# Optimization experiments

Hardware: AMD Instinct MI355X
Metric: run time of the kernel (lower is better)

## Reference

```python
import jax, jax.numpy as jnp
import numpy as np

G_NUMS = 30      # group_nums
G_SIZE = 100     # group_size (also neighborhood_size)
BETA = 1.0
EPS = 1e-9


def setup_inputs() -> dict:
    key = jax.random.key(0)
    pointclouds = jax.random.normal(key, (8, 131072, 3), dtype=jnp.float32)
    return {"pointclouds": pointclouds}


def _knn_gather(points, queries, k):
    """points [b,N,3], queries [b,G,3] -> k nearest points per query [b,G,k,3]."""
    # squared distances [b,G,N]
    d2 = (
        jnp.sum(queries * queries, axis=-1)[..., None]
        - 2.0 * jnp.einsum("bgd,bnd->bgn", queries, points)
        + jnp.sum(points * points, axis=-1)[:, None, :]
    )
    _, idx = jax.lax.top_k(-d2, k)                    # [b,G,k]
    nbrs = jax.vmap(lambda p, i: p[i])(points, idx)   # [b,G,k,3]
    return nbrs


def reference(pointclouds):
    b, N, _ = pointclouds.shape
    # --- group_points: uniform-stride sampled centers, k-NN groups, group means ---
    stride = N // G_NUMS
    centers = pointclouds[:, ::stride][:, :G_NUMS]                 # [b,G,3]
    grouped = _knn_gather(pointclouds, centers, G_SIZE)            # [b,G,K,3]
    group_means = jnp.mean(grouped, axis=2)                        # [b,G,3]

    # --- estimate_pointcloud_local_coord_frames: per-group 3x3 PCA ---
    nbrs = _knn_gather(pointclouds, group_means, G_SIZE)           # [b,G,K,3]
    mu = jnp.mean(nbrs, axis=2, keepdims=True)
    X = nbrs - mu
    cov = jnp.einsum("bgkd,bgke->bgde", X, X) / G_SIZE             # [b,G,3,3]
    curvatures, frames = jnp.linalg.eigh(cov)                      # eigvals ascending

    # --- elongated-shape loss ---
    denom = curvatures[..., 0] + curvatures[..., 1] + curvatures[..., 2] + EPS
    first_vec = curvatures[..., 2] / denom
    second_vec = curvatures[..., 1] / denom
    elongated_shape_loss = -jnp.sum(first_vec - second_vec) / b

    # --- angular smoothness cost over group means / principal directions ---
    dirs = frames[..., :, 2]                                       # [b,G,3] largest-eig direction
    dm = jnp.sum(
        (group_means[:, :, None, :] - group_means[:, None, :, :]) ** 2, axis=-1
    )                                                              # [b,G,G]
    dm = dm + jnp.eye(G_NUMS, dtype=dm.dtype) * jnp.float32(1e30)  # exclude self
    j = jnp.argmin(dm, axis=-1)                                    # [b,G]
    dirs_j = jnp.take_along_axis(dirs, j[..., None], axis=1)       # [b,G,3]
    cos = jnp.sum(dirs * dirs_j, axis=-1)
    dlo_smooth_loss = jnp.mean(1.0 - cos * cos)                    # sign-invariant angle cost

    return elongated_shape_loss + BETA * dlo_smooth_loss
```

## Files before the change

kernel.cpp:

```cpp
#include <hip/hip_runtime.h>
#include <math.h>

#define N_PTS     131072
#define G_NUMS    30
#define G_SIZE    100
#define PT_STRIDE (N_PTS / G_NUMS)
#define TPB       1024
#define NWAVES    (TPB / 64)
#define BINS      4096
#define JB        (BINS / TPB)
#define SHIFT     20
#define SAMPLE_GRPS 1024
#define RANK_CUT  32
#define CAP       3072
#define TIE_CAP   64

struct KSmem {
    union {
        unsigned hist[BINS];
        struct {
            float gm[256][3];
            float dir[256][3];
            float pe[NWAVES];
            float ps[NWAVES];
        } fin;
    };
    unsigned wsum[NWAVES];
    unsigned T;
    int ns, nd, nt;
    unsigned u[CAP];
    int idx[CAP];
    float px[CAP], py[CAP], pz[CAP];
    int sel[G_SIZE];
    unsigned tu[TIE_CAP];
    int ti[TIE_CAP];
    float acc[3], cov[6], q[3];
    unsigned tau0, maxu, r1;
    float delta2;
};

__device__ __forceinline__ float dist2f(float px, float py, float pz,
                                        float qx, float qy, float qz) {
    float dx = px - qx, dy = py - qy, dz = pz - qz;
    return fmaf(dx, dx, fmaf(dy, dy, dz * dz));
}

__device__ __forceinline__ unsigned find_bin(KSmem& sm, unsigned rank,
                                             int tid, int lane, int wid) {
    unsigned hv[JB], csum = 0;
#pragma unroll
    for (int j = 0; j < JB; j++) { hv[j] = sm.hist[tid * JB + j]; csum += hv[j]; }
    unsigned inc = csum;
#pragma unroll
    for (int off = 1; off < 64; off <<= 1) {
        unsigned n = __shfl_up(inc, off);
        if (lane >= off) inc += n;
    }
    __syncthreads();
    if (lane == 63) sm.wsum[wid] = inc;
    __syncthreads();
    unsigned base = 0;
    for (int w = 0; w < wid; w++) base += sm.wsum[w];
    unsigned c = base + inc - csum;
#pragma unroll
    for (int j = 0; j < JB; j++) {
        if (c < rank && c + hv[j] >= rank) sm.T = (unsigned)(tid * JB + j);
        c += hv[j];
    }
    __syncthreads();
    return sm.T;
}

__device__ __forceinline__ void push4(KSmem& sm, const float4& xv, const float4& yv,
                                      const float4& zv, int i, unsigned tau,
                                      float qx, float qy, float qz) {
    unsigned u0 = __float_as_uint(dist2f(xv.x, yv.x, zv.x, qx, qy, qz));
    unsigned u1 = __float_as_uint(dist2f(xv.y, yv.y, zv.y, qx, qy, qz));
    unsigned u2 = __float_as_uint(dist2f(xv.z, yv.z, zv.z, qx, qy, qz));
    unsigned u3 = __float_as_uint(dist2f(xv.w, yv.w, zv.w, qx, qy, qz));
    int i0 = i * 4;
    if (u0 < tau) { int p = atomicAdd(&sm.ns, 1); if (p < CAP) { sm.u[p] = u0; sm.idx[p] = i0;     sm.px[p] = xv.x; sm.py[p] = yv.x; sm.pz[p] = zv.x; } }
    if (u1 < tau) { int p = atomicAdd(&sm.ns, 1); if (p < CAP) { sm.u[p] = u1; sm.idx[p] = i0 + 1; sm.px[p] = xv.y; sm.py[p] = yv.y; sm.pz[p] = zv.y; } }
    if (u2 < tau) { int p = atomicAdd(&sm.ns, 1); if (p < CAP) { sm.u[p] = u2; sm.idx[p] = i0 + 2; sm.px[p] = xv.z; sm.py[p] = yv.z; sm.pz[p] = zv.z; } }
    if (u3 < tau) { int p = atomicAdd(&sm.ns, 1); if (p < CAP) { sm.u[p] = u3; sm.idx[p] = i0 + 3; sm.px[p] = xv.w; sm.py[p] = yv.w; sm.pz[p] = zv.w; } }
}

template<bool SOA>
__device__ void knn_select(const float4* __restrict__ P4,
                           const float4* __restrict__ X4,
                           const float4* __restrict__ Y4,
                           const float4* __restrict__ Z4,
                           KSmem& sm, float qx, float qy, float qz,
                           int tid, int lane, int wid, bool save_tau) {
    for (int j = tid; j < BINS; j += TPB) sm.hist[j] = 0u;
    if (tid == 0) { sm.ns = 0; sm.nd = 0; sm.nt = 0; sm.T = 0u; }
    __syncthreads();

    if constexpr (SOA) {
        for (int i = tid; i < SAMPLE_GRPS; i += TPB) {
            float4 xv = X4[i], yv = Y4[i], zv = Z4[i];
            atomicAdd(&sm.hist[__float_as_uint(dist2f(xv.x, yv.x, zv.x, qx, qy, qz)) >> SHIFT], 1u);
            atomicAdd(&sm.hist[__float_as_uint(dist2f(xv.y, yv.y, zv.y, qx, qy, qz)) >> SHIFT], 1u);
            atomicAdd(&sm.hist[__float_as_uint(dist2f(xv.z, yv.z, zv.z, qx, qy, qz)) >> SHIFT], 1u);
            atomicAdd(&sm.hist[__float_as_uint(dist2f(xv.w, yv.w, zv.w, qx, qy, qz)) >> SHIFT], 1u);
        }
    } else {
        for (int grp = tid; grp < SAMPLE_GRPS; grp += TPB) {
            float4 f0 = P4[3 * grp + 0];
            float4 f1 = P4[3 * grp + 1];
            float4 f2 = P4[3 * grp + 2];
            atomicAdd(&sm.hist[__float_as_uint(dist2f(f0.x, f0.y, f0.z, qx, qy, qz)) >> SHIFT], 1u);
            atomicAdd(&sm.hist[__float_as_uint(dist2f(f0.w, f1.x, f1.y, qx, qy, qz)) >> SHIFT], 1u);
            atomicAdd(&sm.hist[__float_as_uint(dist2f(f1.z, f1.w, f2.x, qx, qy, qz)) >> SHIFT], 1u);
            atomicAdd(&sm.hist[__float_as_uint(dist2f(f2.y, f2.z, f2.w, qx, qy, qz)) >> SHIFT], 1u);
        }
    }
    __syncthreads();
    unsigned Tc = find_bin(sm, RANK_CUT, tid, lane, wid);
    const unsigned tau = (Tc >= BINS - 1) ? 0xFFFFFFFFu : ((Tc + 1) << SHIFT);
    if (save_tau && tid == 0) sm.tau0 = tau;
    for (int j = tid; j < BINS; j += TPB) sm.hist[j] = 0u;
    __syncthreads();

    if constexpr (SOA) {
        for (int base = 0; base < N_PTS / 4; base += TPB * 4) {
            int ia = base + tid, ib = ia + TPB, ic = ib + TPB, id_ = ic + TPB;
            float4 xa = X4[ia], ya = Y4[ia], za = Z4[ia];
            float4 xb = X4[ib], yb = Y4[ib], zb = Z4[ib];
            float4 xc = X4[ic], yc = Y4[ic], zc = Z4[ic];
            float4 xd = X4[id_], yd = Y4[id_], zd = Z4[id_];
            push4(sm, xa, ya, za, ia, tau, qx, qy, qz);
            push4(sm, xb, yb, zb, ib, tau, qx, qy, qz);
            push4(sm, xc, yc, zc, ic, tau, qx, qy, qz);
            push4(sm, xd, yd, zd, id_, tau, qx, qy, qz);
        }
    } else {
#pragma unroll 4
        for (int grp = tid; grp < N_PTS / 4; grp += TPB) {
            float4 f0 = P4[3 * grp + 0];
            float4 f1 = P4[3 * grp + 1];
            float4 f2 = P4[3 * grp + 2];
            float4 xv = make_float4(f0.x, f0.w, f1.z, f2.y);
            float4 yv = make_float4(f0.y, f1.x, f1.w, f2.z);
            float4 zv = make_float4(f0.z, f1.y, f2.x, f2.w);
            push4(sm, xv, yv, zv, grp, tau, qx, qy, qz);
        }
    }
    __syncthreads();
    int S = sm.ns; if (S > CAP) S = CAP;

    unsigned hb = 32u - (unsigned)__clz(tau - 1u);
    unsigned s2 = hb > 12u ? hb - 12u : 0u;
    for (int i = tid; i < S; i += TPB) atomicAdd(&sm.hist[sm.u[i] >> s2], 1u);
    __syncthreads();
    unsigned T2 = find_bin(sm, G_SIZE, tid, lane, wid);
    const unsigned lo = T2 << s2;

    for (int i = tid; i < S; i += TPB) {
        unsigned uu = sm.u[i];
        if (uu < lo) {
            int p = atomicAdd(&sm.nd, 1);
            if (p < G_SIZE) sm.sel[p] = i;
        } else if ((uu >> s2) == T2) {
            int p = atomicAdd(&sm.nt, 1);
            if (p < TIE_CAP) { sm.tu[p] = uu; sm.ti[p] = i; }
        }
    }
    __syncthreads();
    if (tid == 0) {
        int nd = sm.nd; if (nd > G_SIZE) nd = G_SIZE;
        int need = G_SIZE - nd;
        int ec = sm.nt; if (ec > TIE_CAP) ec = TIE_CAP;
        for (int a = 0; a < need && a < ec; ++a) {
            int best = a;
            for (int j = a + 1; j < ec; ++j)
                if (sm.tu[j] < sm.tu[best] ||
                    (sm.tu[j] == sm.tu[best] && sm.idx[sm.ti[j]] < sm.idx[sm.ti[best]])) best = j;
            unsigned tub = sm.tu[best]; sm.tu[best] = sm.tu[a]; sm.tu[a] = tub;
            int tib = sm.ti[best]; sm.ti[best] = sm.ti[a]; sm.ti[a] = tib;
            sm.sel[nd + a] = sm.ti[a];
        }
    }
    __syncthreads();
}

__device__ void eig3(const float cf[6], double lam_out[3], double dir_out[3]) {
    double a[3][3], v[3][3];
    a[0][0] = cf[0]; a[0][1] = cf[1]; a[0][2] = cf[2];
    a[1][0] = cf[1]; a[1][1] = cf[3]; a[1][2] = cf[4];
    a[2][0] = cf[2]; a[2][1] = cf[4]; a[2][2] = cf[5];
    for (int i = 0; i < 3; i++)
        for (int j = 0; j < 3; j++) v[i][j] = (i == j) ? 1.0 : 0.0;

    for (int sweep = 0; sweep < 12; sweep++) {
        double off = a[0][1] * a[0][1] + a[0][2] * a[0][2] + a[1][2] * a[1][2];
        if (off == 0.0) break;
        for (int p = 0; p < 2; p++) {
            for (int q = p + 1; q < 3; q++) {
                double apq = a[p][q];
                if (apq == 0.0) continue;
                double app = a[p][p], aqq = a[q][q];
                double theta = (aqq - app) / (2.0 * apq);
                double t = (theta >= 0.0 ? 1.0 : -1.0) /
                           (fabs(theta) + sqrt(theta * theta + 1.0));
                double c = 1.0 / sqrt(t * t + 1.0);
                double s = t * c;
                a[p][p] = app - t * apq;
                a[q][q] = aqq + t * apq;
                a[p][q] = 0.0; a[q][p] = 0.0;
                for (int r = 0; r < 3; r++) {
                    if (r == p || r == q) continue;
                    double arp = a[r][p], arq = a[r][q];
                    a[r][p] = c * arp - s * arq; a[p][r] = a[r][p];
                    a[r][q] = s * arp + c * arq; a[q][r] = a[r][q];
                }
                for (int r = 0; r < 3; r++) {
                    double vrp = v[r][p], vrq = v[r][q];
                    v[r][p] = c * vrp - s * vrq;
                    v[r][q] = s * vrp + c * vrq;
                }
            }
        }
    }
    double l0 = a[0][0], l1 = a[1][1], l2 = a[2][2];
    int i0 = 0, i1 = 1, i2 = 2;
    if (l0 > l1) { double t = l0; l0 = l1; l1 = t; int ti = i0; i0 = i1; i1 = ti; }
    if (l1 > l2) { double t = l1; l1 = l2; l2 = t; int ti = i1; i1 = i2; i2 = ti; }
    if (l0 > l1) { double t = l0; l0 = l1; l1 = t; int ti = i0; i0 = i1; i1 = ti; }
    lam_out[0] = l0; lam_out[1] = l1; lam_out[2] = l2;
    dir_out[0] = v[0][i2]; dir_out[1] = v[1][i2]; dir_out[2] = v[2][i2];
}

template<bool SOA>
__global__ __launch_bounds__(TPB)
void fused_knn_kernel(const float* __restrict__ pts,
                      const float* __restrict__ sx, const float* __restrict__ sy,
                      const float* __restrict__ sz,
                      float* __restrict__ gmeans, float* __restrict__ covs,
                      float* __restrict__ out,
                      unsigned* __restrict__ syncw,
                      int B, int nblk) {
    __shared__ KSmem sm;
    __shared__ int s_fastok;
    __shared__ int s_last;

    const int blk = blockIdx.x;
    const int b = blk % B;
    const int g = blk / B;
    const int gi = b * G_NUMS + g;
    const float* __restrict__ P = pts + (size_t)b * (N_PTS * 3);
    const float4* __restrict__ P4 = (const float4*)P;
    const float4* X4 = nullptr; const float4* Y4 = nullptr; const float4* Z4 = nullptr;
    if constexpr (SOA) {
        X4 = (const float4*)(sx + (size_t)b * N_PTS);
        Y4 = (const float4*)(sy + (size_t)b * N_PTS);
        Z4 = (const float4*)(sz + (size_t)b * N_PTS);
    }
    const int tid = threadIdx.x;
    const int lane = tid & 63, wid = tid >> 6;

    if (tid == 0) {
        const float* qp = P + (size_t)g * PT_STRIDE * 3;
        sm.q[0] = qp[0]; sm.q[1] = qp[1]; sm.q[2] = qp[2];
    }
    if (tid < 3) sm.acc[tid] = 0.f;
    if (tid < 6) sm.cov[tid] = 0.f;
    __syncthreads();
    const float qx = sm.q[0], qy = sm.q[1], qz = sm.q[2];

    knn_select<SOA>(P4, X4, Y4, Z4, sm, qx, qy, qz, tid, lane, wid, true);

    if (tid < G_SIZE) {
        int p = sm.sel[tid];
        atomicAdd(&sm.acc[0], sm.px[p]);
        atomicAdd(&sm.acc[1], sm.py[p]);
        atomicAdd(&sm.acc[2], sm.pz[p]);
    }
    __syncthreads();
    const int S0 = sm.ns;
    if (tid == 0) {
        float mx = sm.acc[0] * (1.0f / G_SIZE);
        float my = sm.acc[1] * (1.0f / G_SIZE);
        float mz = sm.acc[2] * (1.0f / G_SIZE);
        gmeans[(size_t)gi * 3 + 0] = mx;
        gmeans[(size_t)gi * 3 + 1] = my;
        gmeans[(size_t)gi * 3 + 2] = mz;
        float dx = mx - qx, dy = my - qy, dz = mz - qz;
        sm.delta2 = fmaf(dx, dx, fmaf(dy, dy, dz * dz));
        sm.q[0] = mx; sm.q[1] = my; sm.q[2] = mz;
        sm.acc[0] = 0.f; sm.acc[1] = 0.f; sm.acc[2] = 0.f;
        sm.maxu = 0u; sm.r1 = 0u; sm.T = 0u;
        sm.nd = 0; sm.nt = 0;
        s_last = 0;
        s_fastok = 0;
    }
    __syncthreads();
    const float q1x = sm.q[0], q1y = sm.q[1], q1z = sm.q[2];

    const bool attempt = (S0 >= G_SIZE) && (S0 <= CAP);
    if (attempt) {
        for (int j = tid; j < BINS; j += TPB) sm.hist[j] = 0u;
        for (int i = tid; i < S0; i += TPB) {
            unsigned uu = __float_as_uint(
                dist2f(sm.px[i], sm.py[i], sm.pz[i], q1x, q1y, q1z));
            sm.u[i] = uu;
            atomicMax(&sm.maxu, uu);
        }
        __syncthreads();
        unsigned maxu = sm.maxu;
        unsigned hb = (maxu == 0u) ? 0u : (32u - (unsigned)__clz(maxu));
        unsigned s3 = hb > 12u ? hb - 12u : 0u;
        for (int i = tid; i < S0; i += TPB) atomicAdd(&sm.hist[sm.u[i] >> s3], 1u);
        __syncthreads();
        unsigned T2 = find_bin(sm, G_SIZE, tid, lane, wid);
        const unsigned lo = T2 << s3;
        for (int i = tid; i < S0; i += TPB) {
            unsigned uu = sm.u[i];
            if (uu < lo) {
                int p = atomicAdd(&sm.nd, 1);
                if (p < G_SIZE) sm.sel[p] = i;
            } else if ((uu >> s3) == T2) {
                int p = atomicAdd(&sm.nt, 1);
                if (p < TIE_CAP) { sm.tu[p] = uu; sm.ti[p] = i; }
            }
        }
        __syncthreads();
        if (tid == 0) {
            int ok = 1;
            int nd = sm.nd; if (nd > G_SIZE) { nd = G_SIZE; ok = 0; }
            int need = G_SIZE - nd;
            if (sm.nt > TIE_CAP) ok = 0;
            int ec = sm.nt; if (ec > TIE_CAP) ec = TIE_CAP;
            if (need > ec) ok = 0;
            for (int a = 0; a < need && a < ec; ++a) {
                int best = a;
                for (int j = a + 1; j < ec; ++j)
                    if (sm.tu[j] < sm.tu[best] ||
                        (sm.tu[j] == sm.tu[best] && sm.idx[sm.ti[j]] < sm.idx[sm.ti[best]])) best = j;
                unsigned tub = sm.tu[best]; sm.tu[best] = sm.tu[a]; sm.tu[a] = tub;
                int tib = sm.ti[best]; sm.ti[best] = sm.ti[a]; sm.ti[a] = tib;
                sm.sel[nd + a] = sm.ti[a];
            }
            s_fastok = ok;
        }
        __syncthreads();
        if (s_fastok) {
            if (tid < G_SIZE) atomicMax(&sm.r1, sm.u[sm.sel[tid]]);
            __syncthreads();
            if (tid == 0) {
                double R0 = sqrt((double)__uint_as_float(sm.tau0));
                double dl = sqrt((double)sm.delta2);
                double r1 = sqrt((double)__uint_as_float(sm.r1));
                if (!((R0 - dl) > r1 * 1.0001 + 1e-7)) s_fastok = 0;
            }
            __syncthreads();
        }
    }

    if (!attempt || !s_fastok) {
        knn_select<SOA>(P4, X4, Y4, Z4, sm, q1x, q1y, q1z, tid, lane, wid, false);
    }

    float px = 0.f, py = 0.f, pz = 0.f;
    if (tid < G_SIZE) {
        int p = sm.sel[tid];
        px = sm.px[p]; py = sm.py[p]; pz = sm.pz[p];
        atomicAdd(&sm.acc[0], px);
        atomicAdd(&sm.acc[1], py);
        atomicAdd(&sm.acc[2], pz);
    }
    __syncthreads();
    float mx = sm.acc[0] * (1.0f / G_SIZE);
    float my = sm.acc[1] * (1.0f / G_SIZE);
    float mz = sm.acc[2] * (1.0f / G_SIZE);
    if (tid < G_SIZE) {
        float x = px - mx, y = py - my, z = pz - mz;
        atomicAdd(&sm.cov[0], x * x);
        atomicAdd(&sm.cov[1], x * y);
        atomicAdd(&sm.cov[2], x * z);
        atomicAdd(&sm.cov[3], y * y);
        atomicAdd(&sm.cov[4], y * z);
        atomicAdd(&sm.cov[5], z * z);
    }
    __syncthreads();
    if (tid < 6) covs[(size_t)gi * 6 + tid] = sm.cov[tid] * (1.0f / G_SIZE);

    __syncthreads();
    if (tid == 0) {
        unsigned old = __hip_atomic_fetch_add(&syncw[0], 1u, __ATOMIC_RELEASE,
                                              __HIP_MEMORY_SCOPE_AGENT);
        s_last = (old == (unsigned)(nblk - 1)) ? 1 : 0;
    }
    __syncthreads();
    if (!s_last) return;

    (void)__hip_atomic_load(&syncw[0], __ATOMIC_ACQUIRE, __HIP_MEMORY_SCOPE_AGENT);
    const int NG = nblk;
    float et = 0.f;
    if (tid < NG) {
        float cf[6];
#pragma unroll
        for (int j = 0; j < 6; j++) cf[j] = covs[tid * 6 + j];
        double lam[3], dir[3];
        eig3(cf, lam, dir);
        double denom = lam[0] + lam[1] + lam[2] + 1e-9;
        et = (float)((lam[2] - lam[1]) / denom);
        sm.fin.dir[tid][0] = (float)dir[0];
        sm.fin.dir[tid][1] = (float)dir[1];
        sm.fin.dir[tid][2] = (float)dir[2];
        sm.fin.gm[tid][0] = gmeans[tid * 3 + 0];
        sm.fin.gm[tid][1] = gmeans[tid * 3 + 1];
        sm.fin.gm[tid][2] = gmeans[tid * 3 + 2];
    }
    __syncthreads();

    float st = 0.f;
    if (tid < NG) {
        int bb = tid / G_NUMS, gg0 = tid % G_NUMS;
        float gx = sm.fin.gm[tid][0], gy = sm.fin.gm[tid][1], gz = sm.fin.gm[tid][2];
        float bd = 3.4e38f; int bj = 0;
        for (int gg = 0; gg < G_NUMS; gg++) {
            if (gg == gg0) continue;
            int o = bb * G_NUMS + gg;
            float dx = gx - sm.fin.gm[o][0];
            float dy = gy - sm.fin.gm[o][1];
            float dz = gz - sm.fin.gm[o][2];
            float d = dx * dx + dy * dy + dz * dz;
            if (d < bd) { bd = d; bj = gg; }
        }
        int o = bb * G_NUMS + bj;
        float cosv = sm.fin.dir[tid][0] * sm.fin.dir[o][0] +
                     sm.fin.dir[tid][1] * sm.fin.dir[o][1] +
                     sm.fin.dir[tid][2] * sm.fin.dir[o][2];
        st = 1.f - cosv * cosv;
    }

    float e = et, s2 = st;
#pragma unroll
    for (int off = 32; off > 0; off >>= 1) {
        e += __shfl_down(e, off);
        s2 += __shfl_down(s2, off);
    }
    if (lane == 0) { sm.fin.pe[wid] = e; sm.fin.ps[wid] = s2; }
    __syncthreads();
    if (tid == 0) {
        float se = 0.f, ss = 0.f;
        for (int w = 0; w < NWAVES; w++) { se += sm.fin.pe[w]; ss += sm.fin.ps[w]; }
        out[0] = -se / (float)B + ss / (float)NG;
    }
}

__global__ __launch_bounds__(256)
void transpose_kernel(const float* __restrict__ pts,
                      float* __restrict__ sx, float* __restrict__ sy,
                      float* __restrict__ sz, int total4) {
    int t = blockIdx.x * 256 + threadIdx.x;
    if (t >= total4) return;
    const float4* __restrict__ P4 = (const float4*)pts;
    float4 f0 = P4[3 * t + 0];
    float4 f1 = P4[3 * t + 1];
    float4 f2 = P4[3 * t + 2];
    ((float4*)sx)[t] = make_float4(f0.x, f0.w, f1.z, f2.y);
    ((float4*)sy)[t] = make_float4(f0.y, f1.x, f1.w, f2.z);
    ((float4*)sz)[t] = make_float4(f0.z, f1.y, f2.x, f2.w);
}

extern "C" void kernel_launch(void* const* d_in, const int* in_sizes, int n_in,
                              void* d_out, int out_size, void* d_ws, size_t ws_size,
                              hipStream_t stream) {
    const float* pts = (const float*)d_in[0];
    float* out = (float*)d_out;
    float* ws = (float*)d_ws;
    int B = in_sizes[0] / (N_PTS * 3);
    int nblk = B * G_NUMS;

    float* gmeans = ws;
    float* covs = ws + (size_t)B * G_NUMS * 3;
    const size_t base_floats = (size_t)B * G_NUMS * 9;
    unsigned* syncw = (unsigned*)(ws + base_floats);
    float* soa = ws + base_floats + 16;
    const size_t soa_floats = 3 * (size_t)B * N_PTS;
    const bool use_soa = ws_size >= (base_floats + 16 + soa_floats) * sizeof(float);

    hipMemsetAsync(syncw, 0, 64, stream);

    dim3 grid(nblk);
    if (use_soa) {
        float* sx = soa;
        float* sy = sx + (size_t)B * N_PTS;
        float* sz = sy + (size_t)B * N_PTS;
        int total4 = B * N_PTS / 4;
        transpose_kernel<<<dim3((total4 + 255) / 256), dim3(256), 0, stream>>>(
            pts, sx, sy, sz, total4);
        fused_knn_kernel<true><<<grid, TPB, 0, stream>>>(
            pts, sx, sy, sz, gmeans, covs, out, syncw, B, nblk);
    } else {
        fused_knn_kernel<false><<<grid, TPB, 0, stream>>>(
            pts, nullptr, nullptr, nullptr, gmeans, covs, out, syncw, B, nblk);
    }
}
```

Baseline: 140.1 us.

## Split first kNN pass into chunked multi-query scan kernel plus per-group merge

Replaces the SoA transpose and the per-group full-cloud scan with a scan kernel. Each block loads one chunk of the cloud once, tests it against all 30 centers using thresholds taken from a shared sample, and writes the candidates into fixed-size slabs. A merge kernel then gathers each group's slabs, selects the 100 nearest and runs the second-pass fast path, falling back to a full AoS scan when a slab overflows or the radius check fails. This cuts global point reads from once per query to once per chunk. It costs an extra intermediate buffer and two kernels, and the smaller sample could trigger fallbacks more often. Block size also drops from 1024 to 512 threads.

```diff
diff --git a/kernel.cpp b/kernel.cpp
--- a/kernel.cpp
+++ b/kernel.cpp
@@ -5,15 +5,160 @@
 #define G_NUMS    30
 #define G_SIZE    100
 #define PT_STRIDE (N_PTS / G_NUMS)
-#define TPB       1024
+#define TPB       512
 #define NWAVES    (TPB / 64)
 #define BINS      4096
 #define JB        (BINS / TPB)
 #define SHIFT     20
+
+#define NCHUNK    32
+#define CHUNK     (N_PTS / NCHUNK)
+#define CPT       (CHUNK / TPB)
+#define SMP_N     2048
+#define SMP_PT    (SMP_N / TPB)
+#define SMP_CUT   16
+#define SLAB_CAP  128
+
 #define SAMPLE_GRPS 1024
 #define RANK_CUT  32
 #define CAP       3072
 #define TIE_CAP   64
+
+__device__ __forceinline__ float dist2f(float px, float py, float pz,
+                                        float qx, float qy, float qz) {
+    float dx = px - qx, dy = py - qy, dz = pz - qz;
+    return fmaf(dx, dx, fmaf(dy, dy, dz * dz));
+}
+
+__device__ __forceinline__ unsigned find_bin(unsigned* hist, unsigned* wsum,
+                                             unsigned* T, unsigned rank,
+                                             int tid, int lane, int wid) {
+    unsigned hv[JB], csum = 0;
+#pragma unroll
+    for (int j = 0; j < JB; j++) { hv[j] = hist[tid * JB + j]; csum += hv[j]; }
+    unsigned inc = csum;
+#pragma unroll
+    for (int off = 1; off < 64; off <<= 1) {
+        unsigned n = __shfl_up(inc, off);
+        if (lane >= off) inc += n;
+    }
+    __syncthreads();
+    if (lane == 63) wsum[wid] = inc;
+    __syncthreads();
+    unsigned base = 0;
+    for (int w = 0; w < wid; w++) base += wsum[w];
+    unsigned c = base + inc - csum;
+#pragma unroll
+    for (int j = 0; j < JB; j++) {
+        if (c < rank && c + hv[j] >= rank) *T = (unsigned)(tid * JB + j);
+        c += hv[j];
+    }
+    __syncthreads();
+    return *T;
+}
+
+union ScanU {
+    float    stage[CHUNK * 3];
+    unsigned hist[BINS];
+    uint2    seg[G_NUMS * SLAB_CAP];
+};
+
+__global__ __launch_bounds__(TPB)
+void scan_kernel(const float* __restrict__ pts,
+                 unsigned* __restrict__ taus, unsigned* __restrict__ cnts,
+                 uint2* __restrict__ slabs, unsigned* __restrict__ syncw,
+                 int B) {
+    __shared__ ScanU su;
+    __shared__ float qb[G_NUMS * 3];
+    __shared__ unsigned tau_l[G_NUMS];
+    __shared__ unsigned scnt[G_NUMS];
+    __shared__ unsigned s_wsum[NWAVES];
+    __shared__ unsigned s_T;
+
+    const int b = blockIdx.x % B;
+    const int c = blockIdx.x / B;
+    const float* __restrict__ P = pts + (size_t)b * (N_PTS * 3);
+    const float4* __restrict__ P4 = (const float4*)P;
+    const int tid = threadIdx.x;
+    const int lane = tid & 63, wid = tid >> 6;
+
+    if (blockIdx.x == 0 && tid == 0) syncw[0] = 0;
+
+    if (tid < G_NUMS) {
+        const float* qp = P + (size_t)tid * PT_STRIDE * 3;
+        qb[tid * 3 + 0] = qp[0]; qb[tid * 3 + 1] = qp[1]; qb[tid * 3 + 2] = qp[2];
+        scnt[tid] = 0u;
+    }
+
+    for (int j = tid; j < SMP_N * 3 / 4; j += TPB) ((float4*)su.stage)[j] = P4[j];
+    __syncthreads();
+    float sp[SMP_PT][3];
+#pragma unroll
+    for (int k = 0; k < SMP_PT; k++) {
+        int p = tid + k * TPB;
+        sp[k][0] = su.stage[3 * p + 0];
+        sp[k][1] = su.stage[3 * p + 1];
+        sp[k][2] = su.stage[3 * p + 2];
+    }
+    __syncthreads();
+
+    for (int g = 0; g < G_NUMS; ++g) {
+        for (int j = tid; j < BINS; j += TPB) su.hist[j] = 0u;
+        if (tid == 0) s_T = 0u;
+        __syncthreads();
+        float qx = qb[g * 3 + 0], qy = qb[g * 3 + 1], qz = qb[g * 3 + 2];
+#pragma unroll
+        for (int k = 0; k < SMP_PT; k++) {
+            unsigned d = __float_as_uint(dist2f(sp[k][0], sp[k][1], sp[k][2], qx, qy, qz));
+            atomicAdd(&su.hist[d >> SHIFT], 1u);
+        }
+        __syncthreads();
+        unsigned Tc = find_bin(su.hist, s_wsum, &s_T, SMP_CUT, tid, lane, wid);
+        if (tid == 0)
+            tau_l[g] = (Tc >= BINS - 1) ? 0xFFFFFFFFu : ((Tc + 1) << SHIFT);
+    }
+    __syncthreads();
+
+    const float4* C4 = P4 + (size_t)c * (CHUNK * 3 / 4);
+    for (int j = tid; j < CHUNK * 3 / 4; j += TPB) ((float4*)su.stage)[j] = C4[j];
+    __syncthreads();
+    float cp[CPT][3];
+#pragma unroll
+    for (int k = 0; k < CPT; k++) {
+        int p = tid + k * TPB;
+        cp[k][0] = su.stage[3 * p + 0];
+        cp[k][1] = su.stage[3 * p + 1];
+        cp[k][2] = su.stage[3 * p + 2];
+    }
+    __syncthreads();
+
+    const int ib = c * CHUNK + tid;
+    for (int g = 0; g < G_NUMS; ++g) {
+        float qx = qb[g * 3 + 0], qy = qb[g * 3 + 1], qz = qb[g * 3 + 2];
+        unsigned tau = tau_l[g];
+#pragma unroll
+        for (int k = 0; k < CPT; k++) {
+            unsigned uu = __float_as_uint(dist2f(cp[k][0], cp[k][1], cp[k][2], qx, qy, qz));
+            if (uu < tau) {
+                unsigned p = atomicAdd(&scnt[g], 1u);
+                if (p < SLAB_CAP)
+                    su.seg[g * SLAB_CAP + p] = make_uint2(uu, (unsigned)(ib + k * TPB));
+            }
+        }
+    }
+    __syncthreads();
+
+    for (int e = tid; e < G_NUMS * SLAB_CAP; e += TPB) {
+        int g = e / SLAB_CAP, p = e % SLAB_CAP;
+        unsigned n = scnt[g]; if (n > SLAB_CAP) n = SLAB_CAP;
+        if ((unsigned)p < n)
+            slabs[((size_t)(b * G_NUMS + g) * NCHUNK + c) * SLAB_CAP + p] = su.seg[e];
+    }
+    if (tid < G_NUMS)
+        cnts[(size_t)(b * G_NUMS + tid) * NCHUNK + c] = scnt[tid];
+    if (c == 0 && tid < G_NUMS)
+        taus[b * G_NUMS + tid] = tau_l[tid];
+}
 
 struct KSmem {
     union {
@@ -39,138 +184,84 @@
     float delta2;
 };
 
-__device__ __forceinline__ float dist2f(float px, float py, float pz,
-                                        float qx, float qy, float qz) {
-    float dx = px - qx, dy = py - qy, dz = pz - qz;
-    return fmaf(dx, dx, fmaf(dy, dy, dz * dz));
-}
-
-__device__ __forceinline__ unsigned find_bin(KSmem& sm, unsigned rank,
-                                             int tid, int lane, int wid) {
-    unsigned hv[JB], csum = 0;
-#pragma unroll
-    for (int j = 0; j < JB; j++) { hv[j] = sm.hist[tid * JB + j]; csum += hv[j]; }
-    unsigned inc = csum;
-#pragma unroll
-    for (int off = 1; off < 64; off <<= 1) {
-        unsigned n = __shfl_up(inc, off);
-        if (lane >= off) inc += n;
-    }
-    __syncthreads();
-    if (lane == 63) sm.wsum[wid] = inc;
-    __syncthreads();
-    unsigned base = 0;
-    for (int w = 0; w < wid; w++) base += sm.wsum[w];
-    unsigned c = base + inc - csum;
-#pragma unroll
-    for (int j = 0; j < JB; j++) {
-        if (c < rank && c + hv[j] >= rank) sm.T = (unsigned)(tid * JB + j);
-        c += hv[j];
-    }
-    __syncthreads();
-    return sm.T;
-}
-
-__device__ __forceinline__ void push4(KSmem& sm, const float4& xv, const float4& yv,
-                                      const float4& zv, int i, unsigned tau,
-                                      float qx, float qy, float qz) {
-    unsigned u0 = __float_as_uint(dist2f(xv.x, yv.x, zv.x, qx, qy, qz));
-    unsigned u1 = __float_as_uint(dist2f(xv.y, yv.y, zv.y, qx, qy, qz));
-    unsigned u2 = __float_as_uint(dist2f(xv.z, yv.z, zv.z, qx, qy, qz));
-    unsigned u3 = __float_as_uint(dist2f(xv.w, yv.w, zv.w, qx, qy, qz));
-    int i0 = i * 4;
-    if (u0 < tau) { int p = atomicAdd(&sm.ns, 1); if (p < CAP) { sm.u[p] = u0; sm.idx[p] = i0;     sm.px[p] = xv.x; sm.py[p] = yv.x; sm.pz[p] = zv.x; } }
-    if (u1 < tau) { int p = atomicAdd(&sm.ns, 1); if (p < CAP) { sm.u[p] = u1; sm.idx[p] = i0 + 1; sm.px[p] = xv.y; sm.py[p] = yv.y; sm.pz[p] = zv.y; } }
-    if (u2 < tau) { int p = atomicAdd(&sm.ns, 1); if (p < CAP) { sm.u[p] = u2; sm.idx[p] = i0 + 2; sm.px[p] = xv.z; sm.py[p] = yv.z; sm.pz[p] = zv.z; } }
-    if (u3 < tau) { int p = atomicAdd(&sm.ns, 1); if (p < CAP) { sm.u[p] = u3; sm.idx[p] = i0 + 3; sm.px[p] = xv.w; sm.py[p] = yv.w; sm.pz[p] = zv.w; } }
-}
-
-template<bool SOA>
-__device__ void knn_select(const float4* __restrict__ P4,
-                           const float4* __restrict__ X4,
-                           const float4* __restrict__ Y4,
-                           const float4* __restrict__ Z4,
-                           KSmem& sm, float qx, float qy, float qz,
-                           int tid, int lane, int wid, bool save_tau) {
+__device__ void scan_full_aos(const float4* __restrict__ P4, KSmem& sm,
+                              float qx, float qy, float qz,
+                              int tid, int lane, int wid, bool save_tau) {
     for (int j = tid; j < BINS; j += TPB) sm.hist[j] = 0u;
-    if (tid == 0) { sm.ns = 0; sm.nd = 0; sm.nt = 0; sm.T = 0u; }
-    __syncthreads();
-
-    if constexpr (SOA) {
-        for (int i = tid; i < SAMPLE_GRPS; i += TPB) {
-            float4 xv = X4[i], yv = Y4[i], zv = Z4[i];
-            atomicAdd(&sm.hist[__float_as_uint(dist2f(xv.x, yv.x, zv.x, qx, qy, qz)) >> SHIFT], 1u);
-            atomicAdd(&sm.hist[__float_as_uint(dist2f(xv.y, yv.y, zv.y, qx, qy, qz)) >> SHIFT], 1u);
-            atomicAdd(&sm.hist[__float_as_uint(dist2f(xv.z, yv.z, zv.z, qx, qy, qz)) >> SHIFT], 1u);
-            atomicAdd(&sm.hist[__float_as_uint(dist2f(xv.w, yv.w, zv.w, qx, qy, qz)) >> SHIFT], 1u);
-        }
-    } else {
-        for (int grp = tid; grp < SAMPLE_GRPS; grp += TPB) {
-            float4 f0 = P4[3 * grp + 0];
-            float4 f1 = P4[3 * grp + 1];
-            float4 f2 = P4[3 * grp + 2];
-            atomicAdd(&sm.hist[__float_as_uint(dist2f(f0.x, f0.y, f0.z, qx, qy, qz)) >> SHIFT], 1u);
-            atomicAdd(&sm.hist[__float_as_uint(dist2f(f0.w, f1.x, f1.y, qx, qy, qz)) >> SHIFT], 1u);
-            atomicAdd(&sm.hist[__float_as_uint(dist2f(f1.z, f1.w, f2.x, qx, qy, qz)) >> SHIFT], 1u);
-            atomicAdd(&sm.hist[__float_as_uint(dist2f(f2.y, f2.z, f2.w, qx, qy, qz)) >> SHIFT], 1u);
-        }
-    }
-    __syncthreads();
-    unsigned Tc = find_bin(sm, RANK_CUT, tid, lane, wid);
+    if (tid == 0) { sm.ns = 0; sm.T = 0u; }
+    __syncthreads();
+    for (int grp = tid; grp < SAMPLE_GRPS; grp += TPB) {
+        float4 f0 = P4[3 * grp + 0];
+        float4 f1 = P4[3 * grp + 1];
+        float4 f2 = P4[3 * grp + 2];
+        atomicAdd(&sm.hist[__float_as_uint(dist2f(f0.x, f0.y, f0.z, qx, qy, qz)) >> SHIFT], 1u);
+        atomicAdd(&sm.hist[__float_as_uint(dist2f(f0.w, f1.x, f1.y, qx, qy, qz)) >> SHIFT], 1u);
+        atomicAdd(&sm.hist[__float_as_uint(dist2f(f1.z, f1.w, f2.x, qx, qy, qz)) >> SHIFT], 1u);
+        atomicAdd(&sm.hist[__float_as_uint(dist2f(f2.y, f2.z, f2.w, qx, qy, qz)) >> SHIFT], 1u);
+    }
+    __syncthreads();
+    unsigned Tc = find_bin(sm.hist, sm.wsum, &sm.T, RANK_CUT, tid, lane, wid);
     const unsigned tau = (Tc >= BINS - 1) ? 0xFFFFFFFFu : ((Tc + 1) << SHIFT);
     if (save_tau && tid == 0) sm.tau0 = tau;
+#pragma unroll 4
+    for (int grp = tid; grp < N_PTS / 4; grp += TPB) {
+        float4 f0 = P4[3 * grp + 0];
+        float4 f1 = P4[3 * grp + 1];
+        float4 f2 = P4[3 * grp + 2];
+        float xs[4] = {f0.x, f0.w, f1.z, f2.y};
+        float ys[4] = {f0.y, f1.x, f1.w, f2.z};
+        float zs[4] = {f0.z, f1.y, f2.x, f2.w};
+#pragma unroll
+        for (int k = 0; k < 4; k++) {
+            unsigned uu = __float_as_uint(dist2f(xs[k], ys[k], zs[k], qx, qy, qz));
+            if (uu < tau) {
+                int p = atomicAdd(&sm.ns, 1);
+                if (p < CAP) {
+                    sm.u[p] = uu; sm.idx[p] = grp * 4 + k;
+                    sm.px[p] = xs[k]; sm.py[p] = ys[k]; sm.pz[p] = zs[k];
+                }
+            }
+        }
+    }
+    __syncthreads();
+}
+
+__device__ int select100(KSmem& sm, int* s_flag, int tid, int lane, int wid) {
+    if (tid == 0) { sm.maxu = 0u; sm.nd = 0; sm.nt = 0; sm.T = 0u; *s_flag = 1; }
+    __syncthreads();
+    int S = sm.ns; if (S > CAP) S = CAP;
+    unsigned m = 0;
+    for (int i = tid; i < S; i += TPB) m = max(m, sm.u[i]);
+#pragma unroll
+    for (int off = 32; off > 0; off >>= 1) m = max(m, (unsigned)__shfl_xor((int)m, off));
+    if (lane == 0) atomicMax(&sm.maxu, m);
     for (int j = tid; j < BINS; j += TPB) sm.hist[j] = 0u;
     __syncthreads();
-
-    if constexpr (SOA) {
-        for (int base = 0; base < N_PTS / 4; base += TPB * 4) {
-            int ia = base + tid, ib = ia + TPB, ic = ib + TPB, id_ = ic + TPB;
-            float4 xa = X4[ia], ya = Y4[ia], za = Z4[ia];
-            float4 xb = X4[ib], yb = Y4[ib], zb = Z4[ib];
-            float4 xc = X4[ic], yc = Y4[ic], zc = Z4[ic];
-            float4 xd = X4[id_], yd = Y4[id_], zd = Z4[id_];
-            push4(sm, xa, ya, za, ia, tau, qx, qy, qz);
-            push4(sm, xb, yb, zb, ib, tau, qx, qy, qz);
-            push4(sm, xc, yc, zc, ic, tau, qx, qy, qz);
-            push4(sm, xd, yd, zd, id_, tau, qx, qy, qz);
-        }
-    } else {
-#pragma unroll 4
-        for (int grp = tid; grp < N_PTS / 4; grp += TPB) {
-            float4 f0 = P4[3 * grp + 0];
-            float4 f1 = P4[3 * grp + 1];
-            float4 f2 = P4[3 * grp + 2];
-            float4 xv = make_float4(f0.x, f0.w, f1.z, f2.y);
-            float4 yv = make_float4(f0.y, f1.x, f1.w, f2.z);
-            float4 zv = make_float4(f0.z, f1.y, f2.x, f2.w);
-            push4(sm, xv, yv, zv, grp, tau, qx, qy, qz);
-        }
-    }
-    __syncthreads();
-    int S = sm.ns; if (S > CAP) S = CAP;
-
-    unsigned hb = 32u - (unsigned)__clz(tau - 1u);
-    unsigned s2 = hb > 12u ? hb - 12u : 0u;
-    for (int i = tid; i < S; i += TPB) atomicAdd(&sm.hist[sm.u[i] >> s2], 1u);
-    __syncthreads();
-    unsigned T2 = find_bin(sm, G_SIZE, tid, lane, wid);
-    const unsigned lo = T2 << s2;
-
+    unsigned maxu = sm.maxu;
+    unsigned hb = (maxu == 0u) ? 0u : (32u - (unsigned)__clz(maxu));
+    unsigned s3 = hb > 12u ? hb - 12u : 0u;
+    for (int i = tid; i < S; i += TPB) atomicAdd(&sm.hist[sm.u[i] >> s3], 1u);
+    __syncthreads();
+    unsigned T2 = find_bin(sm.hist, sm.wsum, &sm.T, G_SIZE, tid, lane, wid);
+    const unsigned lo = T2 << s3;
     for (int i = tid; i < S; i += TPB) {
         unsigned uu = sm.u[i];
         if (uu < lo) {
             int p = atomicAdd(&sm.nd, 1);
             if (p < G_SIZE) sm.sel[p] = i;
-        } else if ((uu >> s2) == T2) {
+        } else if ((uu >> s3) == T2) {
             int p = atomicAdd(&sm.nt, 1);
             if (p < TIE_CAP) { sm.tu[p] = uu; sm.ti[p] = i; }
         }
     }
     __syncthreads();
     if (tid == 0) {
+        int bad = 0;
         int nd = sm.nd; if (nd > G_SIZE) nd = G_SIZE;
         int need = G_SIZE - nd;
+        if (sm.nt > TIE_CAP) bad = 1;
         int ec = sm.nt; if (ec > TIE_CAP) ec = TIE_CAP;
+        if (need > ec) bad = 1;
         for (int a = 0; a < need && a < ec; ++a) {
             int best = a;
             for (int j = a + 1; j < ec; ++j)
@@ -180,8 +271,10 @@
             int tib = sm.ti[best]; sm.ti[best] = sm.ti[a]; sm.ti[a] = tib;
             sm.sel[nd + a] = sm.ti[a];
         }
-    }
-    __syncthreads();
+        *s_flag = !bad;
+    }
+    __syncthreads();
+    return *s_flag;
 }
 
 __device__ void eig3(const float cf[6], double lam_out[3], double dir_out[3]) {
@@ -191,7 +284,6 @@
     a[2][0] = cf[2]; a[2][1] = cf[4]; a[2][2] = cf[5];
     for (int i = 0; i < 3; i++)
         for (int j = 0; j < 3; j++) v[i][j] = (i == j) ? 1.0 : 0.0;
-
     for (int sweep = 0; sweep < 12; sweep++) {
         double off = a[0][1] * a[0][1] + a[0][2] * a[0][2] + a[1][2] * a[1][2];
         if (off == 0.0) break;
@@ -231,18 +323,19 @@
     dir_out[0] = v[0][i2]; dir_out[1] = v[1][i2]; dir_out[2] = v[2][i2];
 }
 
-template<bool SOA>
 __global__ __launch_bounds__(TPB)
-void fused_knn_kernel(const float* __restrict__ pts,
-                      const float* __restrict__ sx, const float* __restrict__ sy,
-                      const float* __restrict__ sz,
-                      float* __restrict__ gmeans, float* __restrict__ covs,
-                      float* __restrict__ out,
-                      unsigned* __restrict__ syncw,
-                      int B, int nblk) {
+void merge_kernel(const float* __restrict__ pts,
+                  const unsigned* __restrict__ taus,
+                  const unsigned* __restrict__ cnts,
+                  const uint2* __restrict__ slabs,
+                  float* __restrict__ gmeans, float* __restrict__ covs,
+                  float* __restrict__ out,
+                  unsigned* __restrict__ syncw,
+                  int B, int nblk, int use_slabs) {
     __shared__ KSmem sm;
-    __shared__ int s_fastok;
-    __shared__ int s_last;
+    __shared__ int s_flag, s_ok, s_last, s_fb;
+    __shared__ unsigned s_cnt[NCHUNK];
+    __shared__ int s_pre[NCHUNK];
 
     const int blk = blockIdx.x;
     const int b = blk % B;
@@ -250,25 +343,65 @@
     const int gi = b * G_NUMS + g;
     const float* __restrict__ P = pts + (size_t)b * (N_PTS * 3);
     const float4* __restrict__ P4 = (const float4*)P;
-    const float4* X4 = nullptr; const float4* Y4 = nullptr; const float4* Z4 = nullptr;
-    if constexpr (SOA) {
-        X4 = (const float4*)(sx + (size_t)b * N_PTS);
-        Y4 = (const float4*)(sy + (size_t)b * N_PTS);
-        Z4 = (const float4*)(sz + (size_t)b * N_PTS);
-    }
     const int tid = threadIdx.x;
     const int lane = tid & 63, wid = tid >> 6;
 
     if (tid == 0) {
         const float* qp = P + (size_t)g * PT_STRIDE * 3;
         sm.q[0] = qp[0]; sm.q[1] = qp[1]; sm.q[2] = qp[2];
+        s_fb = !use_slabs;
+        s_last = 0;
     }
     if (tid < 3) sm.acc[tid] = 0.f;
     if (tid < 6) sm.cov[tid] = 0.f;
     __syncthreads();
     const float qx = sm.q[0], qy = sm.q[1], qz = sm.q[2];
 
-    knn_select<SOA>(P4, X4, Y4, Z4, sm, qx, qy, qz, tid, lane, wid, true);
+    if (!s_fb) {
+        if (tid < NCHUNK) s_cnt[tid] = cnts[(size_t)gi * NCHUNK + tid];
+        __syncthreads();
+        if (tid == 0) {
+            int tot = 0, bad = 0;
+            for (int cc = 0; cc < NCHUNK; ++cc) {
+                unsigned n = s_cnt[cc];
+                if (n > SLAB_CAP) bad = 1;
+                s_pre[cc] = tot;
+                tot += (int)(n > SLAB_CAP ? SLAB_CAP : n);
+            }
+            if (tot < G_SIZE || tot > CAP) bad = 1;
+            sm.ns = tot;
+            sm.tau0 = taus[gi];
+            s_fb = bad;
+        }
+        __syncthreads();
+        if (!s_fb) {
+            const uint2* sl = slabs + (size_t)gi * NCHUNK * SLAB_CAP;
+            for (int e = tid; e < NCHUNK * SLAB_CAP; e += TPB) {
+                int cc = e / SLAB_CAP, p = e % SLAB_CAP;
+                unsigned n = s_cnt[cc]; if (n > SLAB_CAP) n = SLAB_CAP;
+                if ((unsigned)p < n) {
+                    uint2 s = sl[e];
+                    int pos = s_pre[cc] + p;
+                    sm.u[pos] = s.x; sm.idx[pos] = (int)s.y;
+                }
+            }
+            __syncthreads();
+            int S = sm.ns;
+            for (int i = tid; i < S; i += TPB) {
+                const float* pp = P + 3 * (size_t)sm.idx[i];
+                sm.px[i] = pp[0]; sm.py[i] = pp[1]; sm.pz[i] = pp[2];
+            }
+            __syncthreads();
+            if (!select100(sm, &s_flag, tid, lane, wid)) {
+                if (tid == 0) s_fb = 1;
+                __syncthreads();
+            }
+        }
+    }
+    if (s_fb) {
+        scan_full_aos(P4, sm, qx, qy, qz, tid, lane, wid, true);
+        select100(sm, &s_flag, tid, lane, wid);
+    }
 
     if (tid < G_SIZE) {
         int p = sm.sel[tid];
@@ -277,7 +410,6 @@
         atomicAdd(&sm.acc[2], sm.pz[p]);
     }
     __syncthreads();
-    const int S0 = sm.ns;
     if (tid == 0) {
         float mx = sm.acc[0] * (1.0f / G_SIZE);
         float my = sm.acc[1] * (1.0f / G_SIZE);
@@ -289,76 +421,31 @@
         sm.delta2 = fmaf(dx, dx, fmaf(dy, dy, dz * dz));
         sm.q[0] = mx; sm.q[1] = my; sm.q[2] = mz;
         sm.acc[0] = 0.f; sm.acc[1] = 0.f; sm.acc[2] = 0.f;
-        sm.maxu = 0u; sm.r1 = 0u; sm.T = 0u;
-        sm.nd = 0; sm.nt = 0;
-        s_last = 0;
-        s_fastok = 0;
+        sm.r1 = 0u;
     }
     __syncthreads();
     const float q1x = sm.q[0], q1y = sm.q[1], q1z = sm.q[2];
 
-    const bool attempt = (S0 >= G_SIZE) && (S0 <= CAP);
-    if (attempt) {
-        for (int j = tid; j < BINS; j += TPB) sm.hist[j] = 0u;
-        for (int i = tid; i < S0; i += TPB) {
-            unsigned uu = __float_as_uint(
-                dist2f(sm.px[i], sm.py[i], sm.pz[i], q1x, q1y, q1z));
-            sm.u[i] = uu;
-            atomicMax(&sm.maxu, uu);
-        }
-        __syncthreads();
-        unsigned maxu = sm.maxu;
-        unsigned hb = (maxu == 0u) ? 0u : (32u - (unsigned)__clz(maxu));
-        unsigned s3 = hb > 12u ? hb - 12u : 0u;
-        for (int i = tid; i < S0; i += TPB) atomicAdd(&sm.hist[sm.u[i] >> s3], 1u);
-        __syncthreads();
-        unsigned T2 = find_bin(sm, G_SIZE, tid, lane, wid);
-        const unsigned lo = T2 << s3;
-        for (int i = tid; i < S0; i += TPB) {
-            unsigned uu = sm.u[i];
-            if (uu < lo) {
-                int p = atomicAdd(&sm.nd, 1);
-                if (p < G_SIZE) sm.sel[p] = i;
-            } else if ((uu >> s3) == T2) {
-                int p = atomicAdd(&sm.nt, 1);
-                if (p < TIE_CAP) { sm.tu[p] = uu; sm.ti[p] = i; }
-            }
-        }
+    {
+        int S = sm.ns; if (S > CAP) S = CAP;
+        for (int i = tid; i < S; i += TPB)
+            sm.u[i] = __float_as_uint(dist2f(sm.px[i], sm.py[i], sm.pz[i], q1x, q1y, q1z));
+        int ok1 = select100(sm, &s_flag, tid, lane, wid);
+        if (tid < G_SIZE) atomicMax(&sm.r1, sm.u[sm.sel[tid]]);
         __syncthreads();
         if (tid == 0) {
-            int ok = 1;
-            int nd = sm.nd; if (nd > G_SIZE) { nd = G_SIZE; ok = 0; }
-            int need = G_SIZE - nd;
-            if (sm.nt > TIE_CAP) ok = 0;
-            int ec = sm.nt; if (ec > TIE_CAP) ec = TIE_CAP;
-            if (need > ec) ok = 0;
-            for (int a = 0; a < need && a < ec; ++a) {
-                int best = a;
-                for (int j = a + 1; j < ec; ++j)
-                    if (sm.tu[j] < sm.tu[best] ||
-                        (sm.tu[j] == sm.tu[best] && sm.idx[sm.ti[j]] < sm.idx[sm.ti[best]])) best = j;
-                unsigned tub = sm.tu[best]; sm.tu[best] = sm.tu[a]; sm.tu[a] = tub;
-                int tib = sm.ti[best]; sm.ti[best] = sm.ti[a]; sm.ti[a] = tib;
-                sm.sel[nd + a] = sm.ti[a];
-            }
-            s_fastok = ok;
+            int ok = ok1;
+            double R0 = sqrt((double)__uint_as_float(sm.tau0));
+            double dl = sqrt((double)sm.delta2);
+            double r1 = sqrt((double)__uint_as_float(sm.r1));
+            if (!((R0 - dl) > r1 * 1.0001 + 1e-7)) ok = 0;
+            s_ok = ok;
         }
         __syncthreads();
-        if (s_fastok) {
-            if (tid < G_SIZE) atomicMax(&sm.r1, sm.u[sm.sel[tid]]);
-            __syncthreads();
-            if (tid == 0) {
-                double R0 = sqrt((double)__uint_as_float(sm.tau0));
-                double dl = sqrt((double)sm.delta2);
-                double r1 = sqrt((double)__uint_as_float(sm.r1));
-                if (!((R0 - dl) > r1 * 1.0001 + 1e-7)) s_fastok = 0;
-            }
-            __syncthreads();
-        }
-    }
-
-    if (!attempt || !s_fastok) {
-        knn_select<SOA>(P4, X4, Y4, Z4, sm, q1x, q1y, q1z, tid, lane, wid, false);
+        if (!s_ok) {
+            scan_full_aos(P4, sm, q1x, q1y, q1z, tid, lane, wid, false);
+            select100(sm, &s_flag, tid, lane, wid);
+        }
     }
 
     float px = 0.f, py = 0.f, pz = 0.f;
@@ -450,21 +537,6 @@
     }
 }
 
-__global__ __launch_bounds__(256)
-void transpose_kernel(const float* __restrict__ pts,
-                      float* __restrict__ sx, float* __restrict__ sy,
-                      float* __restrict__ sz, int total4) {
-    int t = blockIdx.x * 256 + threadIdx.x;
-    if (t >= total4) return;
-    const float4* __restrict__ P4 = (const float4*)pts;
-    float4 f0 = P4[3 * t + 0];
-    float4 f1 = P4[3 * t + 1];
-    float4 f2 = P4[3 * t + 2];
-    ((float4*)sx)[t] = make_float4(f0.x, f0.w, f1.z, f2.y);
-    ((float4*)sy)[t] = make_float4(f0.y, f1.x, f1.w, f2.z);
-    ((float4*)sz)[t] = make_float4(f0.z, f1.y, f2.x, f2.w);
-}
-
 extern "C" void kernel_launch(void* const* d_in, const int* in_sizes, int n_in,
                               void* d_out, int out_size, void* d_ws, size_t ws_size,
                               hipStream_t stream) {
@@ -475,27 +547,22 @@
     int nblk = B * G_NUMS;
 
     float* gmeans = ws;
-    float* covs = ws + (size_t)B * G_NUMS * 3;
-    const size_t base_floats = (size_t)B * G_NUMS * 9;
-    unsigned* syncw = (unsigned*)(ws + base_floats);
-    float* soa = ws + base_floats + 16;
-    const size_t soa_floats = 3 * (size_t)B * N_PTS;
-    const bool use_soa = ws_size >= (base_floats + 16 + soa_floats) * sizeof(float);
-
-    hipMemsetAsync(syncw, 0, 64, stream);
-
-    dim3 grid(nblk);
-    if (use_soa) {
-        float* sx = soa;
-        float* sy = sx + (size_t)B * N_PTS;
-        float* sz = sy + (size_t)B * N_PTS;
-        int total4 = B * N_PTS / 4;
-        transpose_kernel<<<dim3((total4 + 255) / 256), dim3(256), 0, stream>>>(
-            pts, sx, sy, sz, total4);
-        fused_knn_kernel<true><<<grid, TPB, 0, stream>>>(
-            pts, sx, sy, sz, gmeans, covs, out, syncw, B, nblk);
+    float* covs = ws + (size_t)3 * nblk;
+    unsigned* syncw = (unsigned*)(ws + (size_t)9 * nblk);
+    unsigned* taus = syncw + 16;
+    unsigned* cnts = taus + nblk;
+    size_t slab_off_u32 = (size_t)9 * nblk + 16 + nblk + (size_t)nblk * NCHUNK;
+    slab_off_u32 = (slab_off_u32 + 1) & ~(size_t)1;
+    uint2* slabs = (uint2*)((unsigned*)ws + slab_off_u32);
+    size_t need = (slab_off_u32 + (size_t)nblk * NCHUNK * SLAB_CAP * 2) * 4;
+    const int use_slabs = ws_size >= need;
+
+    if (use_slabs) {
+        scan_kernel<<<dim3(B * NCHUNK), dim3(TPB), 0, stream>>>(
+            pts, taus, cnts, slabs, syncw, B);
     } else {
-        fused_knn_kernel<false><<<grid, TPB, 0, stream>>>(
-            pts, nullptr, nullptr, nullptr, gmeans, covs, out, syncw, B, nblk);
-    }
-}
+        hipMemsetAsync(syncw, 0, 64, stream);
+    }
+    merge_kernel<<<dim3(nblk), dim3(TPB), 0, stream>>>(
+        pts, taus, cnts, slabs, gmeans, covs, out, syncw, B, nblk, use_slabs);
+}
```

Result: slower. 182.4 us (+30.3%).
